# Kernel optimization log

Hardware: AMD Instinct MI355X
Metric: run time of the kernel (lower is better)

## Reference

```python
import jax, jax.numpy as jnp
import numpy as np

# model dims (match init_kwargs)
EMBED_DIM = 1024
NUM_HEADS = 16
HEAD_DIM = EMBED_DIM // NUM_HEADS  # 64
WS = 256           # window_size[0]*window_size[1] = 16*16
NW = 64            # number of windows
M = NW * WS        # gathered length = 16384
L = M - 1          # raw tokens (padding row appended makes M rows)
SCALE = HEAD_DIM ** -0.5


def _rope(t, cos, sin):
    # t: [M, H, d]; cos/sin: [M, d] -> broadcast over heads
    c = cos[:, None, :]
    s = sin[:, None, :]
    half = HEAD_DIM // 2
    rot = jnp.concatenate([-t[..., half:], t[..., :half]], axis=-1)
    return t * c + rot * s


def setup_inputs() -> dict:
    key = jax.random.key(0)
    ks = jax.random.split(key, 8)
    x = jax.random.normal(ks[0], (L, EMBED_DIM), jnp.float32)
    # kv_indices: permutation of all M rows (incl. padding row index L) so every
    # token lands in exactly one window slot, as the scatter-back assumes.
    kv_indices = jax.random.permutation(ks[1], M).astype(jnp.int64)
    q_indices = kv_indices            # unused in the manual (non-xformers) branch
    inv_indices = jnp.arange(L, dtype=jnp.int64)  # unused in the manual branch
    # rotary tables over gathered positions
    pos = jnp.arange(M, dtype=jnp.float32)
    inv_freq = 1.0 / (10000.0 ** (jnp.arange(0, HEAD_DIM, 2, dtype=jnp.float32) / HEAD_DIM))
    ang = pos[:, None] * inv_freq[None, :]          # [M, d/2]
    ang = jnp.concatenate([ang, ang], axis=-1)      # [M, d]
    rope_cos = jnp.cos(ang)
    rope_sin = jnp.sin(ang)
    # learned params
    qkv_w = jax.random.normal(ks[2], (3 * EMBED_DIM, EMBED_DIM), jnp.float32) * (EMBED_DIM ** -0.5)
    qkv_b = jax.random.normal(ks[3], (3 * EMBED_DIM,), jnp.float32) * 0.02
    proj_w = jax.random.normal(ks[4], (EMBED_DIM, EMBED_DIM), jnp.float32) * (EMBED_DIM ** -0.5)
    proj_b = jax.random.normal(ks[5], (EMBED_DIM,), jnp.float32) * 0.02
    padding = jnp.zeros((1, EMBED_DIM), jnp.float32)  # nn.Parameter(torch.zeros(1, D))
    return {"x": x, "qkv_w": qkv_w, "qkv_b": qkv_b, "proj_w": proj_w,
            "proj_b": proj_b, "padding": padding, "rope_cos": rope_cos,
            "rope_sin": rope_sin, "kv_indices": kv_indices,
            "q_indices": q_indices, "inv_indices": inv_indices, "ws": WS}


def reference(x, qkv_w, qkv_b, proj_w, proj_b, padding, rope_cos, rope_sin,
              kv_indices, q_indices, inv_indices, ws):
    # append padding row: [L+1, D]
    xp = jnp.concatenate([x, padding], axis=0)
    # fused qkv projection -> [M, 3, H, d]
    qkv = (xp @ qkv_w.T + qkv_b).reshape(-1, 3, NUM_HEADS, HEAD_DIM)
    q, k, v = qkv[:, 0], qkv[:, 1], qkv[:, 2]
    # manual windowed branch: gather q/k/v with kv_indices, RoPE (mode='key') on q and k
    qg = _rope(q[kv_indices], rope_cos, rope_sin)   # [M, H, d]
    kg = _rope(k[kv_indices], rope_cos, rope_sin)
    vg = v[kv_indices]
    nw = M // ws
    qw = qg.reshape(nw, ws, NUM_HEADS, HEAD_DIM)
    kw = kg.reshape(nw, ws, NUM_HEADS, HEAD_DIM)
    vw = vg.reshape(nw, ws, NUM_HEADS, HEAD_DIM)
    attn = jax.nn.softmax(SCALE * jnp.einsum('wind,wjnd->wnij', qw, kw), axis=-1)
    ow = jnp.einsum('wnij,wjnd->wind', attn, vw).reshape(M, NUM_HEADS * HEAD_DIM)
    # scatter back to original token order, drop padding row
    ori = jnp.zeros((M, EMBED_DIM), x.dtype).at[kv_indices].set(ow)
    out = ori[:L] @ proj_w.T + proj_b
    return out
```

## Files before the change

kernel.cpp:

```cpp
#include <hip/hip_runtime.h>
#include <hip/hip_bf16.h>

#define EMBED 1024
#define THREE_EMBED 3072
#define NHEAD 16
#define HDIM 64
#define MTOT 16384
#define LTOT 16383

typedef __attribute__((ext_vector_type(8))) short bf16x8;
typedef __attribute__((ext_vector_type(4))) float f32x4;

__device__ __forceinline__ unsigned short f2b(float f) {
  union { float f; unsigned u; } v; v.f = f;
  unsigned r = v.u + 0x7fffu + ((v.u >> 16) & 1u);
  return (unsigned short)(r >> 16);
}
__device__ __forceinline__ float b2f(unsigned short h) {
  union { unsigned u; float f; } v; v.u = ((unsigned)h) << 16;
  return v.f;
}

__device__ __forceinline__ void gload16(const void* g, void* l) {
  __builtin_amdgcn_global_load_lds(
      (const __attribute__((address_space(1))) void*)g,
      (__attribute__((address_space(3))) void*)l, 16, 0, 0);
}

#define BARRIER() asm volatile("s_barrier" ::: "memory")

__global__ __launch_bounds__(256) void cast_inputs(
    const float* __restrict__ x, const float* __restrict__ padding,
    const float* __restrict__ wq, const int* __restrict__ kvi,
    unsigned short* __restrict__ xb, unsigned short* __restrict__ wqb,
    int* __restrict__ inv)
{
  const int NX = MTOT * EMBED / 8;
  const int NQ = THREE_EMBED * EMBED / 8;
  const int total = NX + NQ;
  int g = blockIdx.x * 256 + threadIdx.x;
  const int stride = gridDim.x * 256;
  for (; g < total + MTOT; g += stride) {
    if (g >= total) {
      int i = g - total;
      inv[kvi[i]] = i;
      continue;
    }
    const float* src;
    unsigned short* dst;
    if (g < NX) {
      size_t e = (size_t)g * 8;
      int row = (int)(e >> 10);
      src = (row < LTOT) ? (x + e) : (padding + (e - (size_t)LTOT * 1024));
      dst = xb + e;
    } else {
      size_t e = (size_t)(g - NX) * 8;
      src = wq + e;
      dst = wqb + e;
    }
    float4 a = *(const float4*)src;
    float4 b = *(const float4*)(src + 4);
    ushort4 u0, u1;
    u0.x = f2b(a.x); u0.y = f2b(a.y); u0.z = f2b(a.z); u0.w = f2b(a.w);
    u1.x = f2b(b.x); u1.y = f2b(b.y); u1.z = f2b(b.z); u1.w = f2b(b.w);
    *(ushort4*)dst = u0;
    *(ushort4*)(dst + 4) = u1;
  }
}

template <int EPI>
__global__ __launch_bounds__(512, 2) void gemm256(
    const unsigned short* __restrict__ A, const unsigned short* __restrict__ B,
    const float* __restrict__ bias, const int* __restrict__ idx,
    unsigned short* __restrict__ outb, float* __restrict__ outf)
{
  __shared__ __align__(16) unsigned short lds[65536];
  const int t = threadIdx.x;
  const int lane = t & 63, wid = t >> 6;
  const int l15 = lane & 15, quad = lane >> 4;
  const int wr = wid >> 2, wc = wid & 3;
  const int bm = blockIdx.x, bn = blockIdx.y;

  const int srow = wid * 8 + (lane >> 3);
  const int scol = ((lane & 7) ^ (lane >> 3)) * 8;
  const unsigned short* gA = A + (size_t)(bm * 256 + srow) * EMBED + scol;
  const unsigned short* gB = B + (size_t)(bn * 256 + srow) * EMBED + scol;

  auto stA = [&](int p, int R0, int kt) {
    const unsigned short* g = gA + (size_t)R0 * EMBED + kt * 64;
    char* d = (char*)lds + p * 32768 + R0 * 128 + wid * 1024;
    gload16(g, d);
    gload16(g + (size_t)64 * EMBED, d + 8192);
  };
  auto stB = [&](int p, int R0, int kt) {
    const unsigned short* g = gB + (size_t)R0 * EMBED + kt * 64;
    char* d = (char*)lds + 65536 + p * 32768 + R0 * 128 + wid * 1024;
    gload16(g, d);
    gload16(g + (size_t)64 * EMBED, d + 8192);
  };

  const int aOff = (wr * 128 + l15) * 64;
  const int bOff = (wc * 64 + l15) * 64;
  const int swz0 = (quad ^ (l15 & 7)) * 8;
  const int swz1 = ((quad + 4) ^ (l15 & 7)) * 8;

  f32x4 acc[8][4];
#pragma unroll
  for (int i = 0; i < 8; ++i)
#pragma unroll
    for (int j = 0; j < 4; ++j) acc[i][j] = (f32x4){0.f, 0.f, 0.f, 0.f};

  stA(0, 0, 0); stA(0, 128, 0); stB(0, 0, 0); stB(0, 128, 0);
  stB(1, 0, 1); stB(1, 128, 1);
  asm volatile("s_waitcnt vmcnt(4)" ::: "memory");
  BARRIER();

#define MFMA16(m0, m1)                                                       \
  do {                                                                       \
    _Pragma("unroll") for (int nt = 0; nt < 4; ++nt)                         \
        acc[m0][nt] = __builtin_amdgcn_mfma_f32_16x16x32_bf16(               \
            a00, b0[nt], acc[m0][nt], 0, 0, 0);                              \
    _Pragma("unroll") for (int nt = 0; nt < 4; ++nt)                         \
        acc[m1][nt] = __builtin_amdgcn_mfma_f32_16x16x32_bf16(               \
            a10, b0[nt], acc[m1][nt], 0, 0, 0);                              \
    _Pragma("unroll") for (int nt = 0; nt < 4; ++nt)                         \
        acc[m0][nt] = __builtin_amdgcn_mfma_f32_16x16x32_bf16(               \
            a01, b1[nt], acc[m0][nt], 0, 0, 0);                              \
    _Pragma("unroll") for (int nt = 0; nt < 4; ++nt)                         \
        acc[m1][nt] = __builtin_amdgcn_mfma_f32_16x16x32_bf16(               \
            a11, b1[nt], acc[m1][nt], 0, 0, 0);                              \
  } while (0)

#define TILE(P, KT, STA, STB, WCNT)                                          \
  {                                                                          \
    const unsigned short* Ab = lds + (P) * 16384 + aOff;                     \
    const unsigned short* Bb = lds + 32768 + (P) * 16384 + bOff;             \
    bf16x8 b0[4], b1[4];                                                     \
    {                                                           \
      _Pragma("unroll") for (int nt = 0; nt < 4; ++nt) {                     \
        b0[nt] = *(const bf16x8*)(Bb + nt * 1024 + swz0);                    \
        b1[nt] = *(const bf16x8*)(Bb + nt * 1024 + swz1);                    \
      }                                                                      \
      bf16x8 a00 = *(const bf16x8*)(Ab + 0 * 1024 + swz0);                   \
      bf16x8 a01 = *(const bf16x8*)(Ab + 0 * 1024 + swz1);                   \
      bf16x8 a10 = *(const bf16x8*)(Ab + 1 * 1024 + swz0);                   \
      bf16x8 a11 = *(const bf16x8*)(Ab + 1 * 1024 + swz1);                   \
      if (STA) stA((P) ^ 1, 0, (KT) + 1);                                    \
      BARRIER();                                                             \
      __builtin_amdgcn_s_setprio(1);                                         \
      MFMA16(0, 1);                                                          \
      __builtin_amdgcn_s_setprio(0);                                         \
      BARRIER();                                                             \
    }                                                                        \
    {                                                           \
      bf16x8 a00 = *(const bf16x8*)(Ab + 2 * 1024 + swz0);                   \
      bf16x8 a01 = *(const bf16x8*)(Ab + 2 * 1024 + swz1);                   \
      bf16x8 a10 = *(const bf16x8*)(Ab + 3 * 1024 + swz0);                   \
      bf16x8 a11 = *(const bf16x8*)(Ab + 3 * 1024 + swz1);                   \
      if (STA) stA((P) ^ 1, 128, (KT) + 1);                                  \
      BARRIER();                                                             \
      __builtin_amdgcn_s_setprio(1);                                         \
      MFMA16(2, 3);                                                          \
      __builtin_amdgcn_s_setprio(0);                                         \
      BARRIER();                                                             \
    }                                                                        \
    {                                                           \
      bf16x8 a00 = *(const bf16x8*)(Ab + 4 * 1024 + swz0);                   \
      bf16x8 a01 = *(const bf16x8*)(Ab + 4 * 1024 + swz1);                   \
      bf16x8 a10 = *(const bf16x8*)(Ab + 5 * 1024 + swz0);                   \
      bf16x8 a11 = *(const bf16x8*)(Ab + 5 * 1024 + swz1);                   \
      if (STB) stB((P), 0, (KT) + 2);                                        \
      BARRIER();                                                             \
      __builtin_amdgcn_s_setprio(1);                                         \
      MFMA16(4, 5);                                                          \
      __builtin_amdgcn_s_setprio(0);                                         \
      BARRIER();                                                             \
    }                                                                        \
    {                                                           \
      bf16x8 a00 = *(const bf16x8*)(Ab + 6 * 1024 + swz0);                   \
      bf16x8 a01 = *(const bf16x8*)(Ab + 6 * 1024 + swz1);                   \
      bf16x8 a10 = *(const bf16x8*)(Ab + 7 * 1024 + swz0);                   \
      bf16x8 a11 = *(const bf16x8*)(Ab + 7 * 1024 + swz1);                   \
      if (STB) stB((P), 128, (KT) + 2);                                      \
      BARRIER();                                                             \
      __builtin_amdgcn_s_setprio(1);                                         \
      MFMA16(6, 7);                                                          \
      __builtin_amdgcn_s_setprio(0);                                         \
      if ((WCNT) == 4) asm volatile("s_waitcnt vmcnt(4)" ::: "memory");      \
      if ((WCNT) == 0) asm volatile("s_waitcnt vmcnt(0)" ::: "memory");      \
      BARRIER();                                                             \
    }                                                                        \
  }

#pragma unroll 1
  for (int t2 = 0; t2 < 7; ++t2) {
    const int kt = t2 * 2;
    TILE(0, kt, 1, 1, 4);
    TILE(1, kt + 1, 1, 1, 4);
  }
  TILE(0, 14, 1, 0, 0);
  TILE(1, 15, 0, 0, -1);
#undef TILE
#undef MFMA16

  float bv[4];
#pragma unroll
  for (int nt = 0; nt < 4; ++nt)
    bv[nt] = bias[bn * 256 + wc * 64 + nt * 16 + l15];
  if constexpr (EPI == 0) {
    const int hh = bn * 4 + wc;
    unsigned short* buf = outb + (size_t)hh * (MTOT * HDIM);
#pragma unroll
    for (int mt = 0; mt < 8; ++mt) {
#pragma unroll
      for (int reg = 0; reg < 4; ++reg) {
        int row = bm * 256 + wr * 128 + mt * 16 + quad * 4 + reg;
        int i = idx[row];
#pragma unroll
        for (int nt = 0; nt < 4; ++nt)
          buf[(size_t)i * HDIM + nt * 16 + l15] =
              f2b(acc[mt][nt][reg] + bv[nt]);
      }
    }
  } else {
    const int col = bn * 256 + wc * 64;
#pragma unroll
    for (int mt = 0; mt < 8; ++mt) {
#pragma unroll
      for (int reg = 0; reg < 4; ++reg) {
        int i = bm * 256 + wr * 128 + mt * 16 + quad * 4 + reg;
        int orow = idx[i];
        if (orow < LTOT) {
#pragma unroll
          for (int nt = 0; nt < 4; ++nt)
            outf[(size_t)orow * EMBED + col + nt * 16 + l15] =
                acc[mt][nt][reg] + bv[nt];
        }
      }
    }
  }
}

__global__ __launch_bounds__(256) void rope_qk(
    const float* __restrict__ rope_cos, const float* __restrict__ rope_sin,
    unsigned short* __restrict__ qkvh)
{
  int g = blockIdx.x * 256 + threadIdx.x;
  int dc = g & 3;
  int i  = (g >> 2) & (MTOT - 1);
  int hh = g >> 16;
  unsigned short* p = qkvh + ((size_t)hh * MTOT + i) * HDIM;
  bf16x8 lo = *(const bf16x8*)(p + dc * 8);
  bf16x8 hi = *(const bf16x8*)(p + 32 + dc * 8);
  const float* cp = rope_cos + (size_t)i * HDIM + dc * 8;
  const float* sp = rope_sin + (size_t)i * HDIM + dc * 8;
  float cl[8], ch[8], sl[8], sh[8];
  *(float4*)(cl)     = *(const float4*)(cp);
  *(float4*)(cl + 4) = *(const float4*)(cp + 4);
  *(float4*)(ch)     = *(const float4*)(cp + 32);
  *(float4*)(ch + 4) = *(const float4*)(cp + 36);
  *(float4*)(sl)     = *(const float4*)(sp);
  *(float4*)(sl + 4) = *(const float4*)(sp + 4);
  *(float4*)(sh)     = *(const float4*)(sp + 32);
  *(float4*)(sh + 4) = *(const float4*)(sp + 36);
  const float sc = (hh < 16) ? 0.125f : 1.0f;
  bf16x8 olo, ohi;
#pragma unroll
  for (int j = 0; j < 8; ++j) {
    float a = b2f((unsigned short)lo[j]);
    float b = b2f((unsigned short)hi[j]);
    olo[j] = (short)f2b((a * cl[j] - b * sl[j]) * sc);
    ohi[j] = (short)f2b((b * ch[j] + a * sh[j]) * sc);
  }
  *(bf16x8*)(p + dc * 8) = olo;
  *(bf16x8*)(p + 32 + dc * 8) = ohi;
}

__global__ __launch_bounds__(256) void cast_w(
    const float* __restrict__ w, unsigned short* __restrict__ wb)
{
  int g = blockIdx.x * 256 + threadIdx.x;
  size_t e = (size_t)g * 8;
  float4 a = *(const float4*)(w + e);
  float4 b = *(const float4*)(w + e + 4);
  ushort4 u0, u1;
  u0.x = f2b(a.x); u0.y = f2b(a.y); u0.z = f2b(a.z); u0.w = f2b(a.w);
  u1.x = f2b(b.x); u1.y = f2b(b.y); u1.z = f2b(b.z); u1.w = f2b(b.w);
  *(ushort4*)(wb + e) = u0;
  *(ushort4*)(wb + e + 4) = u1;
}

__global__ __launch_bounds__(256, 3) void attn(
    const unsigned short* __restrict__ qkvh,
    unsigned short* __restrict__ ow)
{
  __shared__ __align__(16) unsigned short sK[128 * 64];
  __shared__ __align__(16) unsigned short sV[64 * 128];
  __shared__ __align__(16) unsigned short sP[4][16 * 40];

  const int t = threadIdx.x;
  const int lane = t & 63, wid = t >> 6;
  const int l15 = lane & 15, quad = lane >> 4;
  const int wwin = blockIdx.x >> 4;
  const int h = blockIdx.x & 15;

  const unsigned short* Qh = qkvh + (size_t)h * (MTOT * HDIM);
  const unsigned short* Kh = qkvh + (size_t)(16 + h) * (MTOT * HDIM);
  const unsigned short* Vh = qkvh + (size_t)(32 + h) * (MTOT * HDIM);

  f32x4 accO[4][4];
  float mrow[4][4], lrow[4][4];
#pragma unroll
  for (int qt = 0; qt < 4; ++qt) {
#pragma unroll
    for (int nt = 0; nt < 4; ++nt) accO[qt][nt] = (f32x4){0.f, 0.f, 0.f, 0.f};
#pragma unroll
    for (int reg = 0; reg < 4; ++reg) { mrow[qt][reg] = -1e30f; lrow[qt][reg] = 0.f; }
  }

  bf16x8 qa[4][2];
#pragma unroll
  for (int qt = 0; qt < 4; ++qt) {
    int i = wwin * 256 + wid * 64 + qt * 16 + l15;
    const unsigned short* qp = Qh + (size_t)i * HDIM;
    qa[qt][0] = *(const bf16x8*)(qp + quad * 8);
    qa[qt][1] = *(const bf16x8*)(qp + 32 + quad * 8);
  }

  for (int half = 0; half < 2; ++half) {
    __syncthreads();
    {
      int key = t >> 1, hx = t & 1;
      int i = wwin * 256 + half * 128 + key;
      const unsigned short* kp = Kh + (size_t)i * HDIM + hx * 32;
#pragma unroll
      for (int cc = 0; cc < 4; ++cc) {
        int c = hx * 4 + cc;
        uint4 kv = *(const uint4*)(kp + cc * 8);
        *(uint4*)(sK + key * 64 + ((c ^ (key & 7)) * 8)) = kv;
      }
      const unsigned short* vp = Vh + (size_t)i * HDIM + hx * 32;
      int kc3 = key >> 3, k7 = key & 7;
#pragma unroll
      for (int c = 0; c < 4; ++c) {
        bf16x8 va = *(const bf16x8*)(vp + c * 8);
#pragma unroll
        for (int j = 0; j < 8; ++j) {
          int d = hx * 32 + c * 8 + j;
          sV[d * 128 + ((kc3 ^ (d & 7)) * 8) + k7] = (unsigned short)va[j];
        }
      }
    }
    __syncthreads();

#pragma unroll
    for (int qt = 0; qt < 4; ++qt) {
      f32x4 accS[8];
#pragma unroll
      for (int nt = 0; nt < 8; ++nt) accS[nt] = (f32x4){0.f, 0.f, 0.f, 0.f};
#pragma unroll
      for (int ks = 0; ks < 2; ++ks) {
#pragma unroll
        for (int nt = 0; nt < 8; ++nt) {
          int key = nt * 16 + l15;
          bf16x8 bk = *(const bf16x8*)(
              sK + key * 64 + (((ks * 4 + quad) ^ (key & 7)) * 8));
          accS[nt] = __builtin_amdgcn_mfma_f32_16x16x32_bf16(
              qa[qt][ks], bk, accS[nt], 0, 0, 0);
        }
      }
#pragma unroll
      for (int reg = 0; reg < 4; ++reg) {
        float mx = accS[0][reg];
#pragma unroll
        for (int nt = 1; nt < 8; ++nt) mx = fmaxf(mx, accS[nt][reg]);
#pragma unroll
        for (int off = 1; off < 16; off <<= 1)
          mx = fmaxf(mx, __shfl_xor(mx, off, 64));
        float mold = mrow[qt][reg];
        float mnew = fmaxf(mold, mx);
        float alpha = __expf(mold - mnew);
        mrow[qt][reg] = mnew;
        float ls = 0.f;
#pragma unroll
        for (int nt = 0; nt < 8; ++nt) {
          float p = __expf(accS[nt][reg] - mnew);
          accS[nt][reg] = p;
          ls += p;
        }
#pragma unroll
        for (int off = 1; off < 16; off <<= 1) ls += __shfl_xor(ls, off, 64);
        lrow[qt][reg] = lrow[qt][reg] * alpha + ls;
#pragma unroll
        for (int nt = 0; nt < 4; ++nt) accO[qt][nt][reg] *= alpha;
      }
#pragma unroll
      for (int kc = 0; kc < 4; ++kc) {
#pragma unroll
        for (int nt2 = 0; nt2 < 2; ++nt2) {
#pragma unroll
          for (int reg = 0; reg < 4; ++reg) {
            sP[wid][(quad * 4 + reg) * 40 + nt2 * 16 + l15] =
                f2b(accS[kc * 2 + nt2][reg]);
          }
        }
        bf16x8 pa = *(const bf16x8*)(&sP[wid][l15 * 40 + quad * 8]);
#pragma unroll
        for (int nt = 0; nt < 4; ++nt) {
          int d = nt * 16 + l15;
          bf16x8 bv = *(const bf16x8*)(
              sV + d * 128 + (((kc * 4 + quad) ^ (d & 7)) * 8));
          accO[qt][nt] = __builtin_amdgcn_mfma_f32_16x16x32_bf16(
              pa, bv, accO[qt][nt], 0, 0, 0);
        }
      }
    }
  }

  __syncthreads();
  unsigned short* scr = sK + wid * 2048;
  const int rlane = lane >> 3;
  const int clane = (lane & 7) * 8;
#pragma unroll
  for (int qt = 0; qt < 4; ++qt) {
#pragma unroll
    for (int reg = 0; reg < 4; ++reg) {
      float invl = 1.0f / lrow[qt][reg];
      int r = quad * 4 + reg;
#pragma unroll
      for (int nt = 0; nt < 4; ++nt)
        scr[r * 72 + nt * 16 + l15] = f2b(accO[qt][nt][reg] * invl);
    }
#pragma unroll
    for (int rr = 0; rr < 2; ++rr) {
      int row = rr * 8 + rlane;
      bf16x8 vv = *(const bf16x8*)(scr + row * 72 + clane);
      int i = wwin * 256 + wid * 64 + qt * 16 + row;
      *(bf16x8*)(ow + (size_t)i * EMBED + h * HDIM + clane) = vv;
    }
  }
}

extern "C" void kernel_launch(void* const* d_in, const int* in_sizes, int n_in,
                              void* d_out, int out_size, void* d_ws, size_t ws_size,
                              hipStream_t stream) {
  const float* x        = (const float*)d_in[0];
  const float* qkv_w    = (const float*)d_in[1];
  const float* qkv_b    = (const float*)d_in[2];
  const float* proj_w   = (const float*)d_in[3];
  const float* proj_b   = (const float*)d_in[4];
  const float* padding  = (const float*)d_in[5];
  const float* rope_cos = (const float*)d_in[6];
  const float* rope_sin = (const float*)d_in[7];
  const int*   kvi      = (const int*)d_in[8];

  unsigned short* qkvh = (unsigned short*)d_ws;
  unsigned short* R    = (unsigned short*)((char*)d_ws +
                            (size_t)MTOT * THREE_EMBED * 2);
  unsigned short* xb = R;
  unsigned short* ow = R;
  unsigned short* wqb = (unsigned short*)d_out;
  unsigned short* wpb = qkvh;
  int* inv = (int*)((char*)d_out + (size_t)LTOT * EMBED * 4 - (size_t)MTOT * 4);
  float* out = (float*)d_out;

  cast_inputs<<<4096, 256, 0, stream>>>(x, padding, qkv_w, kvi, xb, wqb, inv);
  gemm256<0><<<dim3(64, 12), 512, 0, stream>>>(xb, wqb, qkv_b, inv, qkvh,
                                               nullptr);
  rope_qk<<<8192, 256, 0, stream>>>(rope_cos, rope_sin, qkvh);
  attn<<<dim3(64 * 16), 256, 0, stream>>>(qkvh, ow);
  cast_w<<<512, 256, 0, stream>>>(proj_w, wpb);
  gemm256<1><<<dim3(64, 4), 512, 0, stream>>>(ow, wpb, proj_b, kvi, nullptr,
                                              out);
}
```

Baseline: 401.6 us.

## Fuse RoPE into attention, merge proj weight cast, reorder GEMM MFMA loads

Removes the standalone rope_qk kernel and applies rotary embedding (plus the Q scale) while loading Q into registers and K into shared memory inside the attention kernel. This saves a full read and write pass over Q and K. When the workspace is large enough, the proj weight cast is folded into the first cast kernel, dropping one launch. The GEMM inner tile is also restructured so each A/B fragment feeds a 4x4 MFMA group per k-half, which changes the LDS load pattern. The cost is extra cos/sin global loads inside attention, and the same table values are reread by many heads.

```diff
diff --git a/kernel.cpp b/kernel.cpp
--- a/kernel.cpp
+++ b/kernel.cpp
@@ -31,13 +31,14 @@
 
 __global__ __launch_bounds__(256) void cast_inputs(
     const float* __restrict__ x, const float* __restrict__ padding,
-    const float* __restrict__ wq, const int* __restrict__ kvi,
+    const float* __restrict__ wq, const float* __restrict__ wp,
+    const int* __restrict__ kvi,
     unsigned short* __restrict__ xb, unsigned short* __restrict__ wqb,
-    int* __restrict__ inv)
+    unsigned short* __restrict__ wpb, int* __restrict__ inv, int np)
 {
   const int NX = MTOT * EMBED / 8;
   const int NQ = THREE_EMBED * EMBED / 8;
-  const int total = NX + NQ;
+  const int total = NX + NQ + np;
   int g = blockIdx.x * 256 + threadIdx.x;
   const int stride = gridDim.x * 256;
   for (; g < total + MTOT; g += stride) {
@@ -53,10 +54,14 @@
       int row = (int)(e >> 10);
       src = (row < LTOT) ? (x + e) : (padding + (e - (size_t)LTOT * 1024));
       dst = xb + e;
-    } else {
+    } else if (g < NX + NQ) {
       size_t e = (size_t)(g - NX) * 8;
       src = wq + e;
       dst = wqb + e;
+    } else {
+      size_t e = (size_t)(g - NX - NQ) * 8;
+      src = wp + e;
+      dst = wpb + e;
     }
     float4 a = *(const float4*)src;
     float4 b = *(const float4*)(src + 4);
@@ -115,76 +120,58 @@
   asm volatile("s_waitcnt vmcnt(4)" ::: "memory");
   BARRIER();
 
-#define MFMA16(m0, m1)                                                       \
-  do {                                                                       \
-    _Pragma("unroll") for (int nt = 0; nt < 4; ++nt)                         \
-        acc[m0][nt] = __builtin_amdgcn_mfma_f32_16x16x32_bf16(               \
-            a00, b0[nt], acc[m0][nt], 0, 0, 0);                              \
-    _Pragma("unroll") for (int nt = 0; nt < 4; ++nt)                         \
-        acc[m1][nt] = __builtin_amdgcn_mfma_f32_16x16x32_bf16(               \
-            a10, b0[nt], acc[m1][nt], 0, 0, 0);                              \
-    _Pragma("unroll") for (int nt = 0; nt < 4; ++nt)                         \
-        acc[m0][nt] = __builtin_amdgcn_mfma_f32_16x16x32_bf16(               \
-            a01, b1[nt], acc[m0][nt], 0, 0, 0);                              \
-    _Pragma("unroll") for (int nt = 0; nt < 4; ++nt)                         \
-        acc[m1][nt] = __builtin_amdgcn_mfma_f32_16x16x32_bf16(               \
-            a11, b1[nt], acc[m1][nt], 0, 0, 0);                              \
-  } while (0)
+#define MFMAGRP(MB)                                                          \
+  _Pragma("unroll") for (int m = 0; m < 4; ++m)                              \
+      _Pragma("unroll") for (int n = 0; n < 4; ++n)                          \
+          acc[(MB) + m][n] = __builtin_amdgcn_mfma_f32_16x16x32_bf16(        \
+              a[m], b[n], acc[(MB) + m][n], 0, 0, 0);
 
 #define TILE(P, KT, STA, STB, WCNT)                                          \
   {                                                                          \
     const unsigned short* Ab = lds + (P) * 16384 + aOff;                     \
     const unsigned short* Bb = lds + 32768 + (P) * 16384 + bOff;             \
-    bf16x8 b0[4], b1[4];                                                     \
-    {                                                           \
-      _Pragma("unroll") for (int nt = 0; nt < 4; ++nt) {                     \
-        b0[nt] = *(const bf16x8*)(Bb + nt * 1024 + swz0);                    \
-        b1[nt] = *(const bf16x8*)(Bb + nt * 1024 + swz1);                    \
-      }                                                                      \
-      bf16x8 a00 = *(const bf16x8*)(Ab + 0 * 1024 + swz0);                   \
-      bf16x8 a01 = *(const bf16x8*)(Ab + 0 * 1024 + swz1);                   \
-      bf16x8 a10 = *(const bf16x8*)(Ab + 1 * 1024 + swz0);                   \
-      bf16x8 a11 = *(const bf16x8*)(Ab + 1 * 1024 + swz1);                   \
+    bf16x8 a[4], b[4];                                                       \
+    {                                               \
+      _Pragma("unroll") for (int n = 0; n < 4; ++n)                          \
+          b[n] = *(const bf16x8*)(Bb + n * 1024 + swz0);                     \
+      _Pragma("unroll") for (int m = 0; m < 4; ++m)                          \
+          a[m] = *(const bf16x8*)(Ab + m * 1024 + swz0);                     \
       if (STA) stA((P) ^ 1, 0, (KT) + 1);                                    \
       BARRIER();                                                             \
       __builtin_amdgcn_s_setprio(1);                                         \
-      MFMA16(0, 1);                                                          \
+      MFMAGRP(0);                                                            \
       __builtin_amdgcn_s_setprio(0);                                         \
       BARRIER();                                                             \
     }                                                                        \
-    {                                                           \
-      bf16x8 a00 = *(const bf16x8*)(Ab + 2 * 1024 + swz0);                   \
-      bf16x8 a01 = *(const bf16x8*)(Ab + 2 * 1024 + swz1);                   \
-      bf16x8 a10 = *(const bf16x8*)(Ab + 3 * 1024 + swz0);                   \
-      bf16x8 a11 = *(const bf16x8*)(Ab + 3 * 1024 + swz1);                   \
+    {                                               \
+      _Pragma("unroll") for (int m = 0; m < 4; ++m)                          \
+          a[m] = *(const bf16x8*)(Ab + (4 + m) * 1024 + swz0);               \
       if (STA) stA((P) ^ 1, 128, (KT) + 1);                                  \
       BARRIER();                                                             \
       __builtin_amdgcn_s_setprio(1);                                         \
-      MFMA16(2, 3);                                                          \
+      MFMAGRP(4);                                                            \
       __builtin_amdgcn_s_setprio(0);                                         \
       BARRIER();                                                             \
     }                                                                        \
-    {                                                           \
-      bf16x8 a00 = *(const bf16x8*)(Ab + 4 * 1024 + swz0);                   \
-      bf16x8 a01 = *(const bf16x8*)(Ab + 4 * 1024 + swz1);                   \
-      bf16x8 a10 = *(const bf16x8*)(Ab + 5 * 1024 + swz0);                   \
-      bf16x8 a11 = *(const bf16x8*)(Ab + 5 * 1024 + swz1);                   \
+    {                                               \
+      _Pragma("unroll") for (int n = 0; n < 4; ++n)                          \
+          b[n] = *(const bf16x8*)(Bb + n * 1024 + swz1);                     \
+      _Pragma("unroll") for (int m = 0; m < 4; ++m)                          \
+          a[m] = *(const bf16x8*)(Ab + m * 1024 + swz1);                     \
       if (STB) stB((P), 0, (KT) + 2);                                        \
       BARRIER();                                                             \
       __builtin_amdgcn_s_setprio(1);                                         \
-      MFMA16(4, 5);                                                          \
+      MFMAGRP(0);                                                            \
       __builtin_amdgcn_s_setprio(0);                                         \
       BARRIER();                                                             \
     }                                                                        \
-    {                                                           \
-      bf16x8 a00 = *(const bf16x8*)(Ab + 6 * 1024 + swz0);                   \
-      bf16x8 a01 = *(const bf16x8*)(Ab + 6 * 1024 + swz1);                   \
-      bf16x8 a10 = *(const bf16x8*)(Ab + 7 * 1024 + swz0);                   \
-      bf16x8 a11 = *(const bf16x8*)(Ab + 7 * 1024 + swz1);                   \
+    {                                               \
+      _Pragma("unroll") for (int m = 0; m < 4; ++m)                          \
+          a[m] = *(const bf16x8*)(Ab + (4 + m) * 1024 + swz1);               \
       if (STB) stB((P), 128, (KT) + 2);                                      \
       BARRIER();                                                             \
       __builtin_amdgcn_s_setprio(1);                                         \
-      MFMA16(6, 7);                                                          \
+      MFMAGRP(4);                                                            \
       __builtin_amdgcn_s_setprio(0);                                         \
       if ((WCNT) == 4) asm volatile("s_waitcnt vmcnt(4)" ::: "memory");      \
       if ((WCNT) == 0) asm volatile("s_waitcnt vmcnt(0)" ::: "memory");      \
@@ -201,7 +188,7 @@
   TILE(0, 14, 1, 0, 0);
   TILE(1, 15, 0, 0, -1);
 #undef TILE
-#undef MFMA16
+#undef MFMAGRP
 
   float bv[4];
 #pragma unroll
@@ -239,41 +226,6 @@
       }
     }
   }
-}
-
-__global__ __launch_bounds__(256) void rope_qk(
-    const float* __restrict__ rope_cos, const float* __restrict__ rope_sin,
-    unsigned short* __restrict__ qkvh)
-{
-  int g = blockIdx.x * 256 + threadIdx.x;
-  int dc = g & 3;
-  int i  = (g >> 2) & (MTOT - 1);
-  int hh = g >> 16;
-  unsigned short* p = qkvh + ((size_t)hh * MTOT + i) * HDIM;
-  bf16x8 lo = *(const bf16x8*)(p + dc * 8);
-  bf16x8 hi = *(const bf16x8*)(p + 32 + dc * 8);
-  const float* cp = rope_cos + (size_t)i * HDIM + dc * 8;
-  const float* sp = rope_sin + (size_t)i * HDIM + dc * 8;
-  float cl[8], ch[8], sl[8], sh[8];
-  *(float4*)(cl)     = *(const float4*)(cp);
-  *(float4*)(cl + 4) = *(const float4*)(cp + 4);
-  *(float4*)(ch)     = *(const float4*)(cp + 32);
-  *(float4*)(ch + 4) = *(const float4*)(cp + 36);
-  *(float4*)(sl)     = *(const float4*)(sp);
-  *(float4*)(sl + 4) = *(const float4*)(sp + 4);
-  *(float4*)(sh)     = *(const float4*)(sp + 32);
-  *(float4*)(sh + 4) = *(const float4*)(sp + 36);
-  const float sc = (hh < 16) ? 0.125f : 1.0f;
-  bf16x8 olo, ohi;
-#pragma unroll
-  for (int j = 0; j < 8; ++j) {
-    float a = b2f((unsigned short)lo[j]);
-    float b = b2f((unsigned short)hi[j]);
-    olo[j] = (short)f2b((a * cl[j] - b * sl[j]) * sc);
-    ohi[j] = (short)f2b((b * ch[j] + a * sh[j]) * sc);
-  }
-  *(bf16x8*)(p + dc * 8) = olo;
-  *(bf16x8*)(p + 32 + dc * 8) = ohi;
 }
 
 __global__ __launch_bounds__(256) void cast_w(
@@ -292,6 +244,7 @@
 
 __global__ __launch_bounds__(256, 3) void attn(
     const unsigned short* __restrict__ qkvh,
+    const float* __restrict__ rope_cos, const float* __restrict__ rope_sin,
     unsigned short* __restrict__ ow)
 {
   __shared__ __align__(16) unsigned short sK[128 * 64];
@@ -323,8 +276,26 @@
   for (int qt = 0; qt < 4; ++qt) {
     int i = wwin * 256 + wid * 64 + qt * 16 + l15;
     const unsigned short* qp = Qh + (size_t)i * HDIM;
-    qa[qt][0] = *(const bf16x8*)(qp + quad * 8);
-    qa[qt][1] = *(const bf16x8*)(qp + 32 + quad * 8);
+    const float* cp = rope_cos + (size_t)i * HDIM + quad * 8;
+    const float* sp = rope_sin + (size_t)i * HDIM + quad * 8;
+    bf16x8 qlo = *(const bf16x8*)(qp + quad * 8);
+    bf16x8 qhi = *(const bf16x8*)(qp + 32 + quad * 8);
+    float cl[8], ch[8], sl[8], sh[8];
+    *(float4*)(cl)     = *(const float4*)(cp);
+    *(float4*)(cl + 4) = *(const float4*)(cp + 4);
+    *(float4*)(ch)     = *(const float4*)(cp + 32);
+    *(float4*)(ch + 4) = *(const float4*)(cp + 36);
+    *(float4*)(sl)     = *(const float4*)(sp);
+    *(float4*)(sl + 4) = *(const float4*)(sp + 4);
+    *(float4*)(sh)     = *(const float4*)(sp + 32);
+    *(float4*)(sh + 4) = *(const float4*)(sp + 36);
+#pragma unroll
+    for (int j = 0; j < 8; ++j) {
+      float a = b2f((unsigned short)qlo[j]);
+      float b = b2f((unsigned short)qhi[j]);
+      qa[qt][0][j] = (short)f2b((a * cl[j] - b * sl[j]) * 0.125f);
+      qa[qt][1][j] = (short)f2b((b * ch[j] + a * sh[j]) * 0.125f);
+    }
   }
 
   for (int half = 0; half < 2; ++half) {
@@ -332,22 +303,48 @@
     {
       int key = t >> 1, hx = t & 1;
       int i = wwin * 256 + half * 128 + key;
-      const unsigned short* kp = Kh + (size_t)i * HDIM + hx * 32;
-#pragma unroll
-      for (int cc = 0; cc < 4; ++cc) {
-        int c = hx * 4 + cc;
-        uint4 kv = *(const uint4*)(kp + cc * 8);
-        *(uint4*)(sK + key * 64 + ((c ^ (key & 7)) * 8)) = kv;
+      int k7 = key & 7;
+      const unsigned short* kp = Kh + (size_t)i * HDIM;
+      const float* cp = rope_cos + (size_t)i * HDIM;
+      const float* sp = rope_sin + (size_t)i * HDIM;
+#pragma unroll
+      for (int cc = 0; cc < 2; ++cc) {
+        int dlo = hx * 16 + cc * 8;
+        int dhi = dlo + 32;
+        bf16x8 klo = *(const bf16x8*)(kp + dlo);
+        bf16x8 khi = *(const bf16x8*)(kp + dhi);
+        float cl[8], ch[8], sl[8], sh[8];
+        *(float4*)(cl)     = *(const float4*)(cp + dlo);
+        *(float4*)(cl + 4) = *(const float4*)(cp + dlo + 4);
+        *(float4*)(ch)     = *(const float4*)(cp + dhi);
+        *(float4*)(ch + 4) = *(const float4*)(cp + dhi + 4);
+        *(float4*)(sl)     = *(const float4*)(sp + dlo);
+        *(float4*)(sl + 4) = *(const float4*)(sp + dlo + 4);
+        *(float4*)(sh)     = *(const float4*)(sp + dhi);
+        *(float4*)(sh + 4) = *(const float4*)(sp + dhi + 4);
+        bf16x8 olo, ohi;
+#pragma unroll
+        for (int j = 0; j < 8; ++j) {
+          float a = b2f((unsigned short)klo[j]);
+          float b = b2f((unsigned short)khi[j]);
+          olo[j] = (short)f2b(a * cl[j] - b * sl[j]);
+          ohi[j] = (short)f2b(b * ch[j] + a * sh[j]);
+        }
+        int clo = dlo >> 3;
+        int chi = dhi >> 3;
+        *(uint4*)(sK + key * 64 + ((clo ^ k7) * 8)) = *(uint4*)&olo;
+        *(uint4*)(sK + key * 64 + ((chi ^ k7) * 8)) = *(uint4*)&ohi;
       }
       const unsigned short* vp = Vh + (size_t)i * HDIM + hx * 32;
-      int kc3 = key >> 3, k7 = key & 7;
+      int kc3 = key >> 3;
 #pragma unroll
       for (int c = 0; c < 4; ++c) {
         bf16x8 va = *(const bf16x8*)(vp + c * 8);
 #pragma unroll
         for (int j = 0; j < 8; ++j) {
           int d = hx * 32 + c * 8 + j;
-          sV[d * 128 + ((kc3 ^ (d & 7)) * 8) + k7] = (unsigned short)va[j];
+          sV[d * 128 + ((kc3 ^ (d & 7)) * 8) + (key & 7)] =
+              (unsigned short)va[j];
         }
       }
     }
@@ -454,22 +451,28 @@
   const float* rope_sin = (const float*)d_in[7];
   const int*   kvi      = (const int*)d_in[8];
 
+  const size_t QKVH_B = (size_t)MTOT * THREE_EMBED * 2;
+  const size_t R_B    = (size_t)MTOT * EMBED * 2;
+  const size_t W_B    = (size_t)EMBED * EMBED * 2;
   unsigned short* qkvh = (unsigned short*)d_ws;
-  unsigned short* R    = (unsigned short*)((char*)d_ws +
-                            (size_t)MTOT * THREE_EMBED * 2);
+  unsigned short* R    = (unsigned short*)((char*)d_ws + QKVH_B);
   unsigned short* xb = R;
   unsigned short* ow = R;
   unsigned short* wqb = (unsigned short*)d_out;
-  unsigned short* wpb = qkvh;
+  const bool roomy = ws_size >= QKVH_B + R_B + W_B;
+  unsigned short* wpb = roomy
+      ? (unsigned short*)((char*)d_ws + QKVH_B + R_B)
+      : qkvh;
   int* inv = (int*)((char*)d_out + (size_t)LTOT * EMBED * 4 - (size_t)MTOT * 4);
   float* out = (float*)d_out;
 
-  cast_inputs<<<4096, 256, 0, stream>>>(x, padding, qkv_w, kvi, xb, wqb, inv);
+  cast_inputs<<<4096, 256, 0, stream>>>(
+      x, padding, qkv_w, roomy ? proj_w : nullptr, kvi, xb, wqb, wpb, inv,
+      roomy ? (EMBED * EMBED / 8) : 0);
   gemm256<0><<<dim3(64, 12), 512, 0, stream>>>(xb, wqb, qkv_b, inv, qkvh,
                                                nullptr);
-  rope_qk<<<8192, 256, 0, stream>>>(rope_cos, rope_sin, qkvh);
-  attn<<<dim3(64 * 16), 256, 0, stream>>>(qkvh, ow);
-  cast_w<<<512, 256, 0, stream>>>(proj_w, wpb);
+  attn<<<dim3(64 * 16), 256, 0, stream>>>(qkvh, rope_cos, rope_sin, ow);
+  if (!roomy) cast_w<<<512, 256, 0, stream>>>(proj_w, wpb);
   gemm256<1><<<dim3(64, 4), 512, 0, stream>>>(ow, wpb, proj_b, kvi, nullptr,
                                               out);
 }
```

New measurement: 408.0 us. Within noise of the previous version (+1.6%).
